# Optimization experiments

Measured on AMD Instinct MI355X. Metric: run time of the kernel, lower is better.

The kernel has to match this reference:

```python
import jax, jax.numpy as jnp
import numpy as np

B, D, K, L, C = 1024, 512, 255, 256, 80  # batch, feat, internal nodes, leaves, classes
DEPTH = 8  # complete binary tree: 2^8 = 256 leaves


def _build_res_path():
    # res_path[l, k] = 1 if internal node k is on leaf l's path and leaf goes left,
    # -1 if it goes right, 0 if node k not on the path (matches build_tree_squeeze).
    rp = np.zeros((L, K), dtype=np.int32)
    for leaf in range(L):
        node = 0
        for d in range(DEPTH):
            bit = (leaf >> (DEPTH - 1 - d)) & 1  # 0 -> left, 1 -> right
            rp[leaf, node] = 1 if bit == 0 else -1
            node = 2 * node + 1 + bit
    return jnp.asarray(rp)


def setup_inputs() -> dict:
    key = jax.random.key(0)
    k1, k2, k3, k4 = jax.random.split(key, 4)
    x = jax.random.normal(k1, (B, D), dtype=jnp.float32)
    node_embeddings = jax.random.normal(k2, (K, D), dtype=jnp.float32)
    leaf_W = jax.random.normal(k3, (L * C, D), dtype=jnp.float32) * (1.0 / np.sqrt(D))
    leaf_b = jax.random.normal(k4, (L * C,), dtype=jnp.float32) * 0.01
    res_path = _build_res_path()
    return {"x": x, "node_embeddings": node_embeddings, "leaf_W": leaf_W,
            "leaf_b": leaf_b, "res_path": res_path}


def reference(x, node_embeddings, leaf_W, leaf_b, res_path):
    # L2-normalize node embeddings, cosine-sim routing probabilities
    ne = node_embeddings / jnp.linalg.norm(node_embeddings, axis=-1, keepdims=True)
    node_sim = jax.nn.sigmoid(jnp.einsum('bc,kc->bk', x, ne))  # [B, K]
    # leaf decision logits: Linear(D, L*C) reshaped to [B, L, C]
    leaf_dec = (jnp.einsum('bc,oc->bo', x, leaf_W) + leaf_b).reshape(x.shape[0], L, C)
    left_mask = (res_path == 1)[None]    # [1, L, K]
    right_mask = (res_path == -1)[None]  # [1, L, K]
    ns = node_sim[:, None, :]            # [B, 1, K]
    prob_left = jnp.prod(jnp.where(left_mask, ns, 1.0), axis=-1)        # [B, L]
    prob_right = jnp.prod(jnp.where(right_mask, 1.0 - ns, 1.0), axis=-1)  # [B, L]
    probs = (prob_left * prob_right)[..., None] * leaf_dec  # [B, L, C]
    return probs.sum(axis=1), node_sim
```

## Files before the change

### kernel.cpp

```cpp
#include <hip/hip_runtime.h>
#include <stdint.h>

#define B_  1024
#define D_  512
#define K_  255
#define L_  256
#define C_  80

typedef __attribute__((ext_vector_type(8))) short bf16x8;
typedef __attribute__((ext_vector_type(4))) float f32x4;
typedef __attribute__((ext_vector_type(8))) short short8;

#define GLD(gsrc, ldst) \
  __builtin_amdgcn_global_load_lds((const __attribute__((address_space(1))) void*)(gsrc), \
                                   (__attribute__((address_space(3))) void*)(ldst), 16, 0, 0)

__device__ __forceinline__ short cvt_bf16(float f) {
    unsigned u = __float_as_uint(f);
    u += 0x7FFFu + ((u >> 16) & 1u);
    return (short)(u >> 16);
}

__global__ __launch_bounds__(256) void convert_kernel(const float* __restrict__ w,
                                                      const float* __restrict__ x,
                                                      const float* __restrict__ ne,
                                                      short* __restrict__ wb,
                                                      short* __restrict__ xb,
                                                      short* __restrict__ neb) {
    __shared__ float red[256];
    const int tid = threadIdx.x;
    if (blockIdx.x < 2048) {
        size_t i0 = (size_t)blockIdx.x * 256 + tid;
        const size_t stride = 2048u * 256u;
        for (size_t v = i0; v < 1310720u; v += stride) {
            float4 a = ((const float4*)w)[v * 2];
            float4 b = ((const float4*)w)[v * 2 + 1];
            short8 o;
            o[0] = cvt_bf16(a.x); o[1] = cvt_bf16(a.y); o[2] = cvt_bf16(a.z); o[3] = cvt_bf16(a.w);
            o[4] = cvt_bf16(b.x); o[5] = cvt_bf16(b.y); o[6] = cvt_bf16(b.z); o[7] = cvt_bf16(b.w);
            ((short8*)wb)[v] = o;
        }
        for (size_t v = i0; v < 65536u; v += stride) {
            float4 a = ((const float4*)x)[v * 2];
            float4 b = ((const float4*)x)[v * 2 + 1];
            short8 o;
            o[0] = cvt_bf16(a.x); o[1] = cvt_bf16(a.y); o[2] = cvt_bf16(a.z); o[3] = cvt_bf16(a.w);
            o[4] = cvt_bf16(b.x); o[5] = cvt_bf16(b.y); o[6] = cvt_bf16(b.z); o[7] = cvt_bf16(b.w);
            ((short8*)xb)[v] = o;
        }
    } else {
        const int row = blockIdx.x - 2048;
        if (row == 255) {
            ((unsigned*)(neb + 255 * 512))[tid] = 0u;
            return;
        }
        const float2* nr = (const float2*)(ne + (size_t)row * 512);
        float2 a = nr[tid];
        red[tid] = a.x * a.x + a.y * a.y;
        __syncthreads();
        #pragma unroll
        for (int s = 128; s > 0; s >>= 1) {
            if (tid < s) red[tid] += red[tid + s];
            __syncthreads();
        }
        float inv = rsqrtf(red[0]);
        unsigned lo = (unsigned short)cvt_bf16(a.x * inv);
        unsigned hi = (unsigned short)cvt_bf16(a.y * inv);
        ((unsigned*)(neb + (size_t)row * 512))[tid] = lo | (hi << 16);
    }
}

__global__ __launch_bounds__(256) void simgemm_kernel(const short* __restrict__ xb,
                                                      const short* __restrict__ neb,
                                                      float* __restrict__ out1) {
    __shared__ __align__(16) short Ald[512 * 8];
    __shared__ __align__(16) short Bld[512 * 8];
    const int tid = threadIdx.x;
    const int lane = tid & 63, wave = tid >> 6;
    const int q = lane >> 4, r = lane & 15;
    const int mt = blockIdx.x >> 2;
    const int nt = blockIdx.x & 3;

    f32x4 acc[4];
    #pragma unroll
    for (int nf = 0; nf < 4; ++nf) acc[nf] = (f32x4){0.f, 0.f, 0.f, 0.f};

    const bf16x8* Av = (const bf16x8*)Ald;
    const bf16x8* Bv = (const bf16x8*)Bld;

    for (int kb = 0; kb < 8; ++kb) {
        __syncthreads();
        #pragma unroll
        for (int j = 0; j < 2; ++j) {
            int ph = j * 256 + tid, rr = ph >> 3, g = (ph & 7) ^ (rr & 7);
            GLD(xb + ((size_t)(mt * 64 + rr) * D_ + kb * 64 + g * 8), Ald + ph * 8);
        }
        #pragma unroll
        for (int j = 0; j < 2; ++j) {
            int ph = j * 256 + tid, cc = ph >> 3, g = (ph & 7) ^ (cc & 7);
            GLD(neb + ((size_t)(nt * 64 + cc) * D_ + kb * 64 + g * 8), Bld + ph * 8);
        }
        __syncthreads();
        #pragma unroll
        for (int ks = 0; ks < 2; ++ks) {
            const int g = ks * 4 + q;
            int rl = wave * 16 + r;
            bf16x8 af = Av[rl * 8 + (g ^ (rl & 7))];
            #pragma unroll
            for (int nf = 0; nf < 4; ++nf) {
                int cl = nf * 16 + r;
                bf16x8 bfr = Bv[cl * 8 + (g ^ (cl & 7))];
                acc[nf] = __builtin_amdgcn_mfma_f32_16x16x32_bf16(af, bfr, acc[nf], 0, 0, 0);
            }
        }
    }
    #pragma unroll
    for (int nf = 0; nf < 4; ++nf) {
        int gcol = nt * 64 + nf * 16 + r;
        if (gcol < K_) {
            #pragma unroll
            for (int i = 0; i < 4; ++i) {
                int grow = mt * 64 + wave * 16 + q * 4 + i;
                out1[(size_t)grow * K_ + gcol] = 1.f / (1.f + __expf(-acc[nf][i]));
            }
        }
    }
}

__global__ __launch_bounds__(256) void leafprob_kernel(const float* __restrict__ out1,
                                                       float* __restrict__ p_ws) {
    __shared__ float ss[K_];
    const int b = blockIdx.x, t = threadIdx.x;
    if (t < K_) ss[t] = out1[(size_t)b * K_ + t];
    __syncthreads();
    float prob = 1.f;
    int node = 0;
    #pragma unroll
    for (int d = 0; d < 8; ++d) {
        int bit = (t >> (7 - d)) & 1;
        float s = ss[node];
        prob *= bit ? (1.f - s) : s;
        node = 2 * node + 1 + bit;
    }
    p_ws[(size_t)b * L_ + t] = prob;
}

__global__ __launch_bounds__(256, 4) void gemm_kernel(const short* __restrict__ xb,
                                                      const short* __restrict__ wb,
                                                      const float* __restrict__ p,
                                                      const float* __restrict__ lb,
                                                      float* __restrict__ partial) {
    __shared__ __align__(16) short Ald[1024 * 8];
    __shared__ __align__(16) short Bld[1280 * 8];
    __shared__ float p_ld[128][2];
    __shared__ float b_ld[160];

    const int tid = threadIdx.x;
    const int lane = tid & 63, wave = tid >> 6;
    const int q = lane >> 4, r = lane & 15;
    const int wrow = wave * 32;
    const int lp = blockIdx.x & 127;
    const int mt = blockIdx.x >> 7;

    if (tid < 128) {
        p_ld[tid][0] = p[(size_t)(mt * 128 + tid) * L_ + 2 * lp];
        p_ld[tid][1] = p[(size_t)(mt * 128 + tid) * L_ + 2 * lp + 1];
    }
    if (tid < 160) b_ld[tid] = lb[lp * 160 + tid];

    f32x4 dec[2][10];
    #pragma unroll
    for (int mf = 0; mf < 2; ++mf)
        #pragma unroll
        for (int nf = 0; nf < 10; ++nf)
            dec[mf][nf] = (f32x4){0.f, 0.f, 0.f, 0.f};

    const bf16x8* Av = (const bf16x8*)Ald;
    const bf16x8* Bv = (const bf16x8*)Bld;

    for (int kb = 0; kb < 8; ++kb) {
        __syncthreads();
        #pragma unroll
        for (int j = 0; j < 4; ++j) {
            int ph = j * 256 + tid, rr = ph >> 3, g = (ph & 7) ^ (rr & 7);
            GLD(xb + ((size_t)(mt * 128 + rr) * D_ + kb * 64 + g * 8), Ald + ph * 8);
        }
        #pragma unroll
        for (int j = 0; j < 5; ++j) {
            int ph = j * 256 + tid, cc = ph >> 3, g = (ph & 7) ^ (cc & 7);
            GLD(wb + ((size_t)(lp * 160 + cc) * D_ + kb * 64 + g * 8), Bld + ph * 8);
        }
        __syncthreads();
        #pragma unroll
        for (int ks = 0; ks < 2; ++ks) {
            const int g = ks * 4 + q;
            bf16x8 af[2];
            #pragma unroll
            for (int mf = 0; mf < 2; ++mf) {
                int rl = wrow + mf * 16 + r;
                af[mf] = Av[rl * 8 + (g ^ (rl & 7))];
            }
            #pragma unroll
            for (int half = 0; half < 2; ++half) {
                bf16x8 bfr[5];
                #pragma unroll
                for (int nf = 0; nf < 5; ++nf) {
                    int cl = half * 80 + nf * 16 + r;
                    bfr[nf] = Bv[cl * 8 + (g ^ (cl & 7))];
                }
                #pragma unroll
                for (int mf = 0; mf < 2; ++mf)
                    #pragma unroll
                    for (int nf = 0; nf < 5; ++nf)
                        dec[mf][half * 5 + nf] = __builtin_amdgcn_mfma_f32_16x16x32_bf16(
                            af[mf], bfr[nf], dec[mf][half * 5 + nf], 0, 0, 0);
            }
        }
    }

    const size_t rbase = (size_t)lp * B_ + mt * 128;
    #pragma unroll
    for (int mf = 0; mf < 2; ++mf) {
        #pragma unroll
        for (int nf = 0; nf < 5; ++nf) {
            int c = nf * 16 + r;
            float b0 = b_ld[c], b1 = b_ld[80 + c];
            #pragma unroll
            for (int i = 0; i < 4; ++i) {
                int row = wrow + mf * 16 + q * 4 + i;
                float v = p_ld[row][0] * (dec[mf][nf][i] + b0)
                        + p_ld[row][1] * (dec[mf][nf + 5][i] + b1);
                partial[(rbase + row) * C_ + c] = v;
            }
        }
    }
}

__global__ __launch_bounds__(256) void reduce_kernel(const float* __restrict__ partial,
                                                     float* __restrict__ out0) {
    int idx = blockIdx.x * 256 + threadIdx.x;
    float s = 0.f;
    #pragma unroll 8
    for (int j = 0; j < 128; ++j)
        s += partial[(size_t)j * (B_ * C_) + idx];
    out0[idx] = s;
}

extern "C" void kernel_launch(void* const* d_in, const int* in_sizes, int n_in,
                              void* d_out, int out_size, void* d_ws, size_t ws_size,
                              hipStream_t stream) {
    const float* x  = (const float*)d_in[0];
    const float* ne = (const float*)d_in[1];
    const float* lW = (const float*)d_in[2];
    const float* lb = (const float*)d_in[3];

    float* out0 = (float*)d_out;
    float* out1 = out0 + (size_t)B_ * C_;

    char* ws = (char*)d_ws;
    short* xb      = (short*)ws;
    short* neb     = (short*)(ws + (1u << 20));
    float* p_ws    = (float*)(ws + (1u << 20) + (1u << 18));
    short* wb      = (short*)(ws + (9u << 18));
    float* partial = (float*)(ws + (24u << 20));

    convert_kernel<<<2304, 256, 0, stream>>>(lW, x, ne, wb, xb, neb);
    simgemm_kernel<<<64, 256, 0, stream>>>(xb, neb, out1);
    leafprob_kernel<<<B_, 256, 0, stream>>>(out1, p_ws);
    gemm_kernel<<<1024, 256, 0, stream>>>(xb, wb, p_ws, lb, partial);
    reduce_kernel<<<(B_ * C_) / 256, 256, 0, stream>>>(partial, out0);
}
```

Baseline: 143.1 us.

## Process two leaves sequentially in gemm block and vectorize reduction loads

The leaf GEMM block now loops over its two leaves one at a time. It keeps only 10 accumulators instead of 20 and halves the B tile in shared memory, which lowers register and LDS pressure. The cost is reloading the x tile from global memory for each leaf, so A traffic doubles and the K loop runs twice as often. The reduction kernel now reads and writes float4, with a quarter as many threads.

```diff
diff --git a/kernel.cpp b/kernel.cpp
--- a/kernel.cpp
+++ b/kernel.cpp
@@ -151,7 +151,7 @@
                                                       const float* __restrict__ lb,
                                                       float* __restrict__ partial) {
     __shared__ __align__(16) short Ald[1024 * 8];
-    __shared__ __align__(16) short Bld[1280 * 8];
+    __shared__ __align__(16) short Bld[640 * 8];
     __shared__ float p_ld[128][2];
     __shared__ float b_ld[160];
 
@@ -168,82 +168,110 @@
     }
     if (tid < 160) b_ld[tid] = lb[lp * 160 + tid];
 
-    f32x4 dec[2][10];
+    f32x4 outacc[2][5];
     #pragma unroll
     for (int mf = 0; mf < 2; ++mf)
         #pragma unroll
-        for (int nf = 0; nf < 10; ++nf)
-            dec[mf][nf] = (f32x4){0.f, 0.f, 0.f, 0.f};
+        for (int nf = 0; nf < 5; ++nf)
+            outacc[mf][nf] = (f32x4){0.f, 0.f, 0.f, 0.f};
 
     const bf16x8* Av = (const bf16x8*)Ald;
     const bf16x8* Bv = (const bf16x8*)Bld;
 
-    for (int kb = 0; kb < 8; ++kb) {
-        __syncthreads();
-        #pragma unroll
-        for (int j = 0; j < 4; ++j) {
-            int ph = j * 256 + tid, rr = ph >> 3, g = (ph & 7) ^ (rr & 7);
-            GLD(xb + ((size_t)(mt * 128 + rr) * D_ + kb * 64 + g * 8), Ald + ph * 8);
-        }
-        #pragma unroll
-        for (int j = 0; j < 5; ++j) {
-            int ph = j * 256 + tid, cc = ph >> 3, g = (ph & 7) ^ (cc & 7);
-            GLD(wb + ((size_t)(lp * 160 + cc) * D_ + kb * 64 + g * 8), Bld + ph * 8);
-        }
-        __syncthreads();
-        #pragma unroll
-        for (int ks = 0; ks < 2; ++ks) {
-            const int g = ks * 4 + q;
-            bf16x8 af[2];
-            #pragma unroll
-            for (int mf = 0; mf < 2; ++mf) {
-                int rl = wrow + mf * 16 + r;
-                af[mf] = Av[rl * 8 + (g ^ (rl & 7))];
-            }
-            #pragma unroll
-            for (int half = 0; half < 2; ++half) {
-                bf16x8 bfr[5];
+    for (int li = 0; li < 2; ++li) {
+        const int l = lp * 2 + li;
+        f32x4 dec[2][5];
+        #pragma unroll
+        for (int mf = 0; mf < 2; ++mf)
+            #pragma unroll
+            for (int nf = 0; nf < 5; ++nf)
+                dec[mf][nf] = (f32x4){0.f, 0.f, 0.f, 0.f};
+
+        for (int kb = 0; kb < 8; ++kb) {
+            __syncthreads();
+            #pragma unroll
+            for (int j = 0; j < 4; ++j) {
+                int ph = j * 256 + tid;
+                int rr = ph >> 3;
+                int g  = (ph & 7) ^ (rr & 7);
+                GLD(xb + ((size_t)(mt * 128 + rr) * D_ + kb * 64 + g * 8), Ald + ph * 8);
+            }
+            #pragma unroll
+            for (int j = 0; j < 2; ++j) {
+                int ph = j * 256 + tid;
+                int cc = ph >> 3;
+                int g  = (ph & 7) ^ (cc & 7);
+                GLD(wb + ((size_t)(l * C_ + cc) * D_ + kb * 64 + g * 8), Bld + ph * 8);
+            }
+            if (tid < 128) {
+                int ph = 512 + tid;
+                int cc = ph >> 3;
+                int g  = (ph & 7) ^ (cc & 7);
+                GLD(wb + ((size_t)(l * C_ + cc) * D_ + kb * 64 + g * 8), Bld + ph * 8);
+            }
+            __syncthreads();
+
+            #pragma unroll
+            for (int ks = 0; ks < 2; ++ks) {
+                const int g = ks * 4 + q;
+                bf16x8 af[2], bfr[5];
+                #pragma unroll
+                for (int mf = 0; mf < 2; ++mf) {
+                    int rl = wrow + mf * 16 + r;
+                    af[mf] = Av[rl * 8 + (g ^ (rl & 7))];
+                }
                 #pragma unroll
                 for (int nf = 0; nf < 5; ++nf) {
-                    int cl = half * 80 + nf * 16 + r;
+                    int cl = nf * 16 + r;
                     bfr[nf] = Bv[cl * 8 + (g ^ (cl & 7))];
                 }
                 #pragma unroll
                 for (int mf = 0; mf < 2; ++mf)
                     #pragma unroll
                     for (int nf = 0; nf < 5; ++nf)
-                        dec[mf][half * 5 + nf] = __builtin_amdgcn_mfma_f32_16x16x32_bf16(
-                            af[mf], bfr[nf], dec[mf][half * 5 + nf], 0, 0, 0);
+                        dec[mf][nf] = __builtin_amdgcn_mfma_f32_16x16x32_bf16(
+                            af[mf], bfr[nf], dec[mf][nf], 0, 0, 0);
+            }
+        }
+
+        #pragma unroll
+        for (int mf = 0; mf < 2; ++mf) {
+            #pragma unroll
+            for (int nf = 0; nf < 5; ++nf) {
+                float bv = b_ld[li * 80 + nf * 16 + r];
+                #pragma unroll
+                for (int i = 0; i < 4; ++i) {
+                    int row = wrow + mf * 16 + q * 4 + i;
+                    outacc[mf][nf][i] += p_ld[row][li] * (dec[mf][nf][i] + bv);
+                }
             }
         }
     }
 
     const size_t rbase = (size_t)lp * B_ + mt * 128;
     #pragma unroll
-    for (int mf = 0; mf < 2; ++mf) {
-        #pragma unroll
-        for (int nf = 0; nf < 5; ++nf) {
-            int c = nf * 16 + r;
-            float b0 = b_ld[c], b1 = b_ld[80 + c];
+    for (int mf = 0; mf < 2; ++mf)
+        #pragma unroll
+        for (int nf = 0; nf < 5; ++nf)
             #pragma unroll
             for (int i = 0; i < 4; ++i) {
                 int row = wrow + mf * 16 + q * 4 + i;
-                float v = p_ld[row][0] * (dec[mf][nf][i] + b0)
-                        + p_ld[row][1] * (dec[mf][nf + 5][i] + b1);
-                partial[(rbase + row) * C_ + c] = v;
-            }
-        }
-    }
+                int col = nf * 16 + r;
+                partial[(rbase + row) * C_ + col] = outacc[mf][nf][i];
+            }
 }
 
 __global__ __launch_bounds__(256) void reduce_kernel(const float* __restrict__ partial,
                                                      float* __restrict__ out0) {
     int idx = blockIdx.x * 256 + threadIdx.x;
-    float s = 0.f;
+    const float4* p4 = (const float4*)partial;
+    float4 s = {0.f, 0.f, 0.f, 0.f};
     #pragma unroll 8
-    for (int j = 0; j < 128; ++j)
-        s += partial[(size_t)j * (B_ * C_) + idx];
-    out0[idx] = s;
+    for (int j = 0; j < 128; ++j) {
+        float4 v = p4[(size_t)j * (B_ * C_ / 4) + idx];
+        s.x += v.x; s.y += v.y; s.z += v.z; s.w += v.w;
+    }
+    ((float4*)out0)[idx] = s;
 }
 
 extern "C" void kernel_launch(void* const* d_in, const int* in_sizes, int n_in,
@@ -268,5 +296,5 @@
     simgemm_kernel<<<64, 256, 0, stream>>>(xb, neb, out1);
     leafprob_kernel<<<B_, 256, 0, stream>>>(out1, p_ws);
     gemm_kernel<<<1024, 256, 0, stream>>>(xb, wb, p_ws, lb, partial);
-    reduce_kernel<<<(B_ * C_) / 256, 256, 0, stream>>>(partial, out0);
-}
+    reduce_kernel<<<B_ * C_ / 1024, 256, 0, stream>>>(partial, out0);
+}
```

Result: slower. 187.5 us (+31.0%).
